# Optimization experiments

Hardware: AMD Instinct MI355X
Metric: run time of the kernel (lower is better)

The kernel has to match this reference:

```python
import jax, jax.numpy as jnp
import numpy as np

EPS = 1e-8  # `eps` is an undefined global in the original repo snippet; standard capsule eps
CH_J, N_J, R_NUM = 32, 4, 3


def _squash(s):
    # Faithful to the source: norm / (1 + norm^2 + eps) * s, norm over last dim (size 1 here)
    norm = jnp.sqrt(jnp.sum(s * s, axis=-1, keepdims=True))
    return norm / (1.0 + norm ** 2 + EPS) * s


def _unif_act_wt_entropy(k):
    # k: (b, W, W, 1, ch_j, ch_i); softmax was taken over (W, W, ch_j) per (b, ch_i).
    # Entropy of coupling coefficients normalized by uniform entropy, averaged.
    b, ci = k.shape[0], k.shape[-1]
    p = jnp.transpose(k, (0, 5, 3, 1, 2, 4)).reshape(b, ci, -1)
    ent = -jnp.sum(p * jnp.log(p + EPS), axis=-1)
    return jnp.mean(ent / jnp.log(jnp.asarray(p.shape[-1], p.dtype)))


def reference(inputs, conv_w, conv_b):
    b, ch_i, n_i, h, w = inputs.shape
    # (b, 1, ch_i*n_i, h, w) -> Conv3d stride (n_i,1,1), pad (0,1,1)
    x = inputs.reshape(b, 1, ch_i * n_i, h, w)
    x = jax.lax.conv_general_dilated(
        x, conv_w, window_strides=(n_i, 1, 1),
        padding=((0, 0), (1, 1), (1, 1)),
        dimension_numbers=('NCDHW', 'OIDHW', 'NCDHW'))
    x = x + conv_b[None, :, None, None, None]
    W = x.shape[-1]
    # (b, ch_i, ch_j*n_j, W, W) -> (b, W, W, n_j, ch_j, ch_i)
    x = jnp.transpose(x, (0, 2, 1, 3, 4)).reshape(b, ch_i, CH_J, N_J, W, W)
    x = jnp.transpose(x, (0, 4, 5, 3, 2, 1))

    B = jnp.zeros((b, W, W, 1, CH_J, ch_i), dtype=x.dtype)
    S_hat = None
    k = None
    for i in range(R_NUM):
        # softmax over (W, W, ch_j) jointly, per (b, ch_i)
        logits = jnp.transpose(B, (0, 5, 3, 1, 2, 4)).reshape(b, ch_i, 1, -1)
        k = jax.nn.softmax(logits, axis=-1)
        k = jnp.transpose(k.reshape(b, ch_i, 1, W, W, CH_J), (0, 3, 4, 2, 5, 1))
        S = jnp.sum(k * x, axis=-1, keepdims=True)  # (b, W, W, n_j, ch_j, 1)
        S_hat = _squash(S)
        if i < R_NUM - 1:
            B = B + jnp.sum(S_hat * x, axis=3, keepdims=True)

    out = jnp.transpose(S_hat[..., 0], (0, 4, 3, 1, 2))  # (b, ch_j, n_j, W, W)
    return out, _unif_act_wt_entropy(k)


def setup_inputs() -> dict:
    key = jax.random.key(0)
    k1, k2, k3 = jax.random.split(key, 3)
    inputs = jax.random.normal(k1, (8, 32, 8, 32, 32), dtype=jnp.float32)
    conv_w = jax.random.normal(k2, (128, 1, 3, 3, 3), dtype=jnp.float32) * 0.05
    conv_b = jax.random.normal(k3, (128,), dtype=jnp.float32) * 0.05
    return {"inputs": inputs, "conv_w": conv_w, "conv_b": conv_b}
```

## Files before the change

### kernel.cpp

```cpp
#include <hip/hip_runtime.h>
#include <hip/hip_bf16.h>

#define EPSF 1e-8f

typedef short bf16x8 __attribute__((ext_vector_type(8)));
typedef float f32x4 __attribute__((ext_vector_type(4)));


__device__ __forceinline__ float bflo(unsigned u){ return __uint_as_float(u<<16); }
__device__ __forceinline__ float bfhi(unsigned u){ return __uint_as_float(u&0xffff0000u); }
__device__ __forceinline__ float bfu16(unsigned short u){ return __uint_as_float((unsigned)u<<16); }
__device__ __forceinline__ unsigned bfpack2(float a,float b){
    return (__float_as_uint(a)>>16)|(__float_as_uint(b)&0xffff0000u);
}
__device__ __forceinline__ unsigned short bfr16(float a){
    return (unsigned short)(__float_as_uint(a)>>16);
}
__device__ __forceinline__ float fastrcp(float x){ return __builtin_amdgcn_rcpf(x); }
__device__ __forceinline__ bf16x8 pack8(const float* v){
    union { unsigned u[4]; bf16x8 v8; } cv;
#pragma unroll
    for (int j = 0; j < 4; ++j) cv.u[j] = bfpack2(v[2*j], v[2*j+1]);
    return cv.v8;
}

template<int PHASE>
__global__ __launch_bounds__(256, 5) void k_caps(
    const float* __restrict__ in, const float* __restrict__ cw,
    const float* __restrict__ cb, unsigned* __restrict__ Bpk,
    const float* __restrict__ sm_in, const float* __restrict__ siz_in,
    float* __restrict__ pm, float* __restrict__ ps, float* __restrict__ pt,
    float* __restrict__ outp) {
    __shared__ __align__(16) unsigned char smem[29568];
    unsigned short* slabB = (unsigned short*)smem;
    unsigned short* wLT = (unsigned short*)(smem + 6912);
    float* cbL  = (float*)(smem + 14336);
    float* smL  = (float*)(smem + 14848);
    float* sizL = (float*)(smem + 14976);
    unsigned* ktab = (unsigned*)(smem + 15104);

    const int t = threadIdx.x;
    const int lane = t & 63, wid = t >> 6;
    const int bid = blockIdx.x;
    const int bh = bid >> 3, b = bh >> 5, h = bh & 31;
    const int w0 = (bid & 7) << 2;
    const int l15 = lane & 15, lq = lane >> 4;

    unsigned char* wb = smem + 15232 + (size_t)wid * 3584;
    unsigned* Bu  = (unsigned*)wb;
    float* shL    = (float*)(wb + 2560);
    float* auxL   = (float*)(wb + 3072);
    float* statb  = (float*)(wb + 3200);

    for (int j = t; j < 864; j += 256) {
        const int r = j / 3, q = j - r * 3;
        const int ci2 = r / 9, rem = r - ci2 * 9, kd = rem / 3, dy = rem - kd * 3;
        const int y = h + dy - 1;
        const int x0 = w0 - 4 + q * 4;
        float4 f = {0.f, 0.f, 0.f, 0.f};
        if ((unsigned)y < 32u && (unsigned)x0 < 32u)
            f = *reinterpret_cast<const float4*>(
                in + (((size_t)(b * 32 + ci2) * 8 + kd) * 32 + y) * 32 + x0);
        unsigned* sp = (unsigned*)slabB + r * 6 + q * 2;
        sp[0] = bfpack2(f.x, f.y);
        sp[1] = bfpack2(f.z, f.w);
    }
    for (int j = t; j < 3456; j += 256) {
        const int c = j / 27, k = j - c * 27;
        wLT[k * 132 + c] = bfr16(cw[j]);
    }
    if (t < 128) cbL[t] = cb[t];
    if (t < 32) {
        const int k = t < 27 ? t : 26;
        const int kd = k / 9, r9 = k - kd * 9, dy = r9 / 3, dx = r9 - dy * 3;
        ktab[t] = (unsigned)((kd * 3 + dy) * 12 + dx);
    }
    if constexpr (PHASE >= 1) {
        if (t < 32) { smL[t] = sm_in[b * 32 + t]; sizL[t] = siz_in[b * 32 + t]; }
    }
    __syncthreads();

    const size_t loc = (size_t)bh * 32 + w0 + wid;
    const int tb = wid + 3;

    float b1v[16];
    if constexpr (PHASE == 0) {
        const int k2 = lane >> 1, half = lane & 1;
        float vs = 0.f;
        if (k2 < 27) {
            const unsigned short* sp = slabB + half * 16 * 108 + ktab[k2] + tb;
#pragma unroll
            for (int i = 0; i < 16; ++i) vs += bfu16(sp[i * 108]);
        }
        vs += __shfl_xor(vs, 1);
        if (half == 0 && k2 < 27) auxL[k2] = vs;
    } else {
        const uint4* Bg = (const uint4*)(Bpk + loc * 512 + (size_t)lane * 8);
        const uint4 q0 = Bg[0], q1 = Bg[1];
        const unsigned pk[8] = {q0.x, q0.y, q0.z, q0.w, q1.x, q1.y, q1.z, q1.w};
#pragma unroll
        for (int e = 0; e < 8; ++e) { b1v[2*e] = bflo(pk[e]); b1v[2*e+1] = bfhi(pk[e]); }
#pragma unroll
        for (int mt = 0; mt < 2; ++mt)
#pragma unroll
        for (int reg = 0; reg < 4; ++reg)
#pragma unroll
        for (int nt = 0; nt < 2; ++nt) {
            const float me = b1v[mt*8 + nt*4 + reg];
            const float ot = __shfl_xor(me, 1);
            const unsigned pku = (l15 & 1) ? bfpack2(ot, me) : bfpack2(me, ot);
            if ((l15 & 1) == nt)
                Bu[(mt*16 + lq*4 + reg)*20 + nt*8 + (l15 >> 1)] = pku;
        }
        bf16x8 kmA[2];
#pragma unroll
        for (int mt = 0; mt < 2; ++mt) {
            const uint4 q = *(const uint4*)(Bu + (mt*16 + l15)*20 + lq*4);
            const unsigned uu[4] = {q.x, q.y, q.z, q.w};
            float ev[8];
#pragma unroll
            for (int j2 = 0; j2 < 4; ++j2) {
                const int ci0 = lq*8 + 2*j2;
                ev[2*j2]   = __expf(bflo(uu[j2]) - smL[ci0])   * sizL[ci0];
                ev[2*j2+1] = __expf(bfhi(uu[j2]) - smL[ci0+1]) * sizL[ci0+1];
            }
            kmA[mt] = pack8(ev);
        }
        bf16x8 vtB[2];
#pragma unroll
        for (int nt = 0; nt < 2; ++nt) {
            const int kt = nt*16 + l15;
            const unsigned ko = ktab[kt];
            union { unsigned short s[8]; bf16x8 v8; } cv;
#pragma unroll
            for (int j = 0; j < 8; ++j) {
                const unsigned short sv = slabB[(lq*8 + j)*108 + ko + tb];
                cv.s[j] = (kt < 27) ? sv : (unsigned short)(kt == 27 ? 0x3f80 : 0);
            }
            vtB[nt] = cv.v8;
        }
        f32x4 accu[2][2];
#pragma unroll
        for (int mt = 0; mt < 2; ++mt)
#pragma unroll
        for (int nt = 0; nt < 2; ++nt)
            accu[mt][nt] = __builtin_amdgcn_mfma_f32_16x16x32_bf16(
                kmA[mt], vtB[nt], (f32x4){0.f,0.f,0.f,0.f}, 0, 0, 0);
#pragma unroll
        for (int mt = 0; mt < 2; ++mt)
#pragma unroll
        for (int reg = 0; reg < 4; ++reg)
#pragma unroll
        for (int nt = 0; nt < 2; ++nt) {
            const float me = accu[mt][nt][reg];
            const float ot = __shfl_xor(me, 1);
            const unsigned pku = (l15 & 1) ? bfpack2(ot, me) : bfpack2(me, ot);
            if ((l15 & 1) == nt)
                Bu[(mt*16 + lq*4 + reg)*20 + nt*8 + (l15 >> 1)] = pku;
        }
    }

#pragma unroll
    for (int cc = 0; cc < 2; ++cc) {
        const int c = lane + cc * 64;
        float S;
        if constexpr (PHASE == 0) {
            S = 0.f;
#pragma unroll
            for (int k = 0; k < 27; ++k)
                S = fmaf(bfu16(wLT[k*132 + c]), auxL[k], S);
            S = S * (1.0f/32768.0f) + cbL[c] * (1.0f/1024.0f);
        } else {
            const unsigned* up = Bu + (c >> 2) * 20;
            S = 0.f;
#pragma unroll
            for (int p = 0; p < 13; ++p) {
                const unsigned u = up[p];
                S = fmaf(bfu16(wLT[(2*p)*132 + c]),   bflo(u), S);
                S = fmaf(bfu16(wLT[(2*p+1)*132 + c]), bfhi(u), S);
            }
            const unsigned u13 = up[13];
            S = fmaf(bfu16(wLT[26*132 + c]), bflo(u13), S);
            S = fmaf(cbL[c], bfhi(u13), S);
        }
        const float sq = fabsf(S) * S * fastrcp(1.f + S*S + EPSF);
        shL[c] = sq;
    }

    if constexpr (PHASE == 2) {
        __syncthreads();
        if (t < 128) {
            const float* s0 = (const float*)(smem + 15232 + 0*3584 + 2560);
            const float* s1 = (const float*)(smem + 15232 + 1*3584 + 2560);
            const float* s2 = (const float*)(smem + 15232 + 2*3584 + 2560);
            const float* s3 = (const float*)(smem + 15232 + 3*3584 + 2560);
            float4 o = make_float4(s0[t], s1[t], s2[t], s3[t]);
            *reinterpret_cast<float4*>(
                outp + ((size_t)(b*128 + t))*1024 + (size_t)h*32 + w0) = o;
        }
        if (bid == 0) {
            float* er = (float*)smem;
            er[t] = pt[t];
            __syncthreads();
            for (int s2v = 128; s2v > 0; s2v >>= 1) {
                if (t < s2v) er[t] += er[t + s2v];
                __syncthreads();
            }
            if (t == 0) outp[1048576] = er[0] * (1.0f/256.0f);
        }
        return;
    }

    {
        const int k0 = 2*l15, k1 = k0 + 1;
#pragma unroll
        for (int i = 0; i < 8; ++i) {
            const int cj = lq + 4*i;
            float v0 = 0.f, v1 = 0.f;
            if (k0 < 27) {
#pragma unroll
                for (int nj = 0; nj < 4; ++nj)
                    v0 = fmaf(shL[cj*4+nj], bfu16(wLT[k0*132 + cj*4 + nj]), v0);
            }
            if (k1 < 27) {
#pragma unroll
                for (int nj = 0; nj < 4; ++nj)
                    v1 = fmaf(shL[cj*4+nj], bfu16(wLT[k1*132 + cj*4 + nj]), v1);
            }
            Bu[cj*20 + l15] = bfpack2(v0, v1);
        }
        if (lane < 32) {
            float cv = 0.f;
#pragma unroll
            for (int nj = 0; nj < 4; ++nj)
                cv = fmaf(shL[lane*4+nj], cbL[lane*4+nj], cv);
            auxL[lane] = cv;
        }
    }

    bf16x8 wsA[2], vB[2];
#pragma unroll
    for (int mt = 0; mt < 2; ++mt) {
        union { uint4 q4; bf16x8 v8; } cv;
        cv.q4 = *(const uint4*)(Bu + (mt*16 + l15)*20 + lq*4);
        wsA[mt] = cv.v8;
    }
#pragma unroll
    for (int nt = 0; nt < 2; ++nt) {
        const int ci = nt*16 + l15;
        union { unsigned short s[8]; bf16x8 v8; } cv;
#pragma unroll
        for (int j = 0; j < 8; ++j) {
            const int k = lq*8 + j;
            const unsigned short sv = slabB[ci*108 + ktab[k] + tb];
            cv.s[j] = (k < 27) ? sv : (unsigned short)0;
        }
        vB[nt] = cv.v8;
    }
    f32x4 accb[2][2];
#pragma unroll
    for (int mt = 0; mt < 2; ++mt)
#pragma unroll
    for (int nt = 0; nt < 2; ++nt)
        accb[mt][nt] = __builtin_amdgcn_mfma_f32_16x16x32_bf16(
            wsA[mt], vB[nt], (f32x4){0.f,0.f,0.f,0.f}, 0, 0, 0);

    float bnew[16];
#pragma unroll
    for (int mt = 0; mt < 2; ++mt)
#pragma unroll
    for (int nt = 0; nt < 2; ++nt)
#pragma unroll
    for (int reg = 0; reg < 4; ++reg) {
        float val = accb[mt][nt][reg] + auxL[mt*16 + lq*4 + reg];
        if constexpr (PHASE == 1) val += b1v[mt*8 + nt*4 + reg];
        bnew[mt*8 + nt*4 + reg] = val;
    }
    {
        unsigned pk[8];
#pragma unroll
        for (int e = 0; e < 8; ++e) pk[e] = bfpack2(bnew[2*e], bnew[2*e+1]);
        uint4* Bg = (uint4*)(Bpk + loc * 512 + (size_t)lane * 8);
        Bg[0] = make_uint4(pk[0], pk[1], pk[2], pk[3]);
        Bg[1] = make_uint4(pk[4], pk[5], pk[6], pk[7]);
    }
    float m2[2], s2[2], T2[2];
#pragma unroll
    for (int nt = 0; nt < 2; ++nt) {
        float m = -1e30f;
#pragma unroll
        for (int mt = 0; mt < 2; ++mt)
#pragma unroll
        for (int reg = 0; reg < 4; ++reg) m = fmaxf(m, bnew[mt*8 + nt*4 + reg]);
        float s = 0.f, T = 0.f;
#pragma unroll
        for (int mt = 0; mt < 2; ++mt)
#pragma unroll
        for (int reg = 0; reg < 4; ++reg) {
            const float d = bnew[mt*8 + nt*4 + reg] - m;
            const float e = __expf(d);
            s += e; T += e * d;
        }
        m2[nt] = m; s2[nt] = s; T2[nt] = T;
#pragma unroll
        for (int off = 16; off <= 32; off <<= 1) {
            const float mo = __shfl_xor(m2[nt], off);
            const float so = __shfl_xor(s2[nt], off);
            const float To = __shfl_xor(T2[nt], off);
            const float nm = fmaxf(m2[nt], mo);
            const float ea = __expf(m2[nt]-nm), eb = __expf(mo-nm);
            T2[nt] = ea*(T2[nt] + s2[nt]*(m2[nt]-nm)) + eb*(To + so*(mo-nm));
            s2[nt] = ea*s2[nt] + eb*so;
            m2[nt] = nm;
        }
    }
    if (lane < 16) {
#pragma unroll
        for (int nt = 0; nt < 2; ++nt) {
            const int ci = nt*16 + lane;
            statb[ci] = m2[nt]; statb[32+ci] = s2[nt]; statb[64+ci] = T2[nt];
        }
    }
    __syncthreads();
    if (t < 32) {
        float M = -1e30f, Z = 0.f, T = 0.f;
#pragma unroll
        for (int wv = 0; wv < 4; ++wv) {
            const float* sw = (const float*)(smem + 15232 + wv*3584 + 3200);
            const float mo = sw[t], so = sw[32+t], To = sw[64+t];
            const float nm = fmaxf(M, mo);
            const float ea = __expf(M-nm), eb = __expf(mo-nm);
            T = ea*(T + Z*(M-nm)) + eb*(To + so*(mo-nm));
            Z = ea*Z + eb*so;
            M = nm;
        }
        pm[bid*32 + t] = M;
        ps[bid*32 + t] = Z;
        if constexpr (PHASE == 1) pt[bid*32 + t] = T;
    }
}

template <int NPART, bool ENT>
__global__ __launch_bounds__(256) void k_comb(const float* __restrict__ pm,
                                              const float* __restrict__ ps,
                                              const float* __restrict__ pt,
                                              float* __restrict__ sm,
                                              float* __restrict__ siz,
                                              float* __restrict__ entp) {
    const int b = blockIdx.x, t = threadIdx.x;
    const int ci = t & 31, seg = t >> 5;
    constexpr int PER = NPART / 8;
    __shared__ float red[3][8][33];

    float M = -1e30f;
    for (int k = 0; k < PER; ++k)
        M = fmaxf(M, pm[((size_t)b * NPART + seg * PER + k) * 32 + ci]);
    red[0][seg][ci] = M;
    __syncthreads();
    float Mg = red[0][0][ci];
#pragma unroll
    for (int q = 1; q < 8; ++q) Mg = fmaxf(Mg, red[0][q][ci]);

    float Z = 0.0f, T = 0.0f;
    for (int k = 0; k < PER; ++k) {
        const size_t i = ((size_t)b * NPART + seg * PER + k) * 32 + ci;
        const float dm = pm[i] - Mg;
        const float e = __expf(dm);
        Z += ps[i] * e;
        if constexpr (ENT) T += (pt[i] + ps[i] * dm) * e;
    }
    red[1][seg][ci] = Z;
    if constexpr (ENT) red[2][seg][ci] = T;
    __syncthreads();
    if (t < 32) {
        float Zt = 0.0f, Tt = 0.0f;
#pragma unroll
        for (int q = 0; q < 8; ++q) {
            Zt += red[1][q][ci];
            if constexpr (ENT) Tt += red[2][q][ci];
        }
        sm[b * 32 + ci] = Mg;
        siz[b * 32 + ci] = 1.0f / Zt;
        if constexpr (ENT)
            entp[b * 32 + ci] = (logf(Zt) - Tt / Zt) * (1.0f / 10.39720770839918f);
    }
}

extern "C" void kernel_launch(void* const* d_in, const int* in_sizes, int n_in,
                              void* d_out, int out_size, void* d_ws, size_t ws_size,
                              hipStream_t stream) {
    const float* in = (const float*)d_in[0];
    const float* cw = (const float*)d_in[1];
    const float* cb = (const float*)d_in[2];
    float* out = (float*)d_out;

    unsigned* Bpk = (unsigned*)d_ws;
    float* pm0  = (float*)(Bpk + 4194304);
    float* ps0  = pm0 + 65536;
    float* pm1  = ps0 + 65536;
    float* ps1  = pm1 + 65536;
    float* pt1  = ps1 + 65536;
    float* sm0  = pt1 + 65536;
    float* siz0 = sm0 + 256;
    float* sm1  = siz0 + 256;
    float* siz1 = sm1 + 256;
    float* entp = siz1 + 256;

    k_caps<0><<<2048, 256, 0, stream>>>(in, cw, cb, Bpk, sm0, siz0, pm0, ps0, pt1, out);
    k_comb<256, false><<<8, 256, 0, stream>>>(pm0, ps0, nullptr, sm0, siz0, nullptr);
    k_caps<1><<<2048, 256, 0, stream>>>(in, cw, cb, Bpk, sm0, siz0, pm1, ps1, pt1, out);
    k_comb<256, true><<<8, 256, 0, stream>>>(pm1, ps1, pt1, sm1, siz1, entp);
    k_caps<2><<<2048, 256, 0, stream>>>(in, cw, cb, Bpk, sm1, siz1, pm1, ps1, entp, out);
}
```

Before: 85.61 us.

## Fold softmax-stat combine kernels into caps phases and widen tiles to 8 columns

Removes the two small k_comb launches by having each k_caps phase reduce the previous phase's per-block partial max/sum statistics itself at block start. Each block now covers 8 output columns (two per wave, looped) instead of 4, so the grid halves, the slab is wider and the number of partials per batch halves. Phase 2 computes the entropy from the raw partials in block 0. The intent is to cut launch and serialization overhead and to amortize slab and weight staging over more work. In exchange every block repeats the combine reduction, LDS use grows, and per-wave work is serialized over two columns.

```diff
diff --git a/kernel.cpp b/kernel.cpp
--- a/kernel.cpp
+++ b/kernel.cpp
@@ -28,32 +28,61 @@
 __global__ __launch_bounds__(256, 5) void k_caps(
     const float* __restrict__ in, const float* __restrict__ cw,
     const float* __restrict__ cb, unsigned* __restrict__ Bpk,
-    const float* __restrict__ sm_in, const float* __restrict__ siz_in,
-    float* __restrict__ pm, float* __restrict__ ps, float* __restrict__ pt,
+    const float* __restrict__ pmi, const float* __restrict__ psi,
+    const float* __restrict__ pti,
+    float* __restrict__ pmo, float* __restrict__ pso, float* __restrict__ pto,
     float* __restrict__ outp) {
-    __shared__ __align__(16) unsigned char smem[29568];
+    __shared__ __align__(16) unsigned char smem[31872];
     unsigned short* slabB = (unsigned short*)smem;
-    unsigned short* wLT = (unsigned short*)(smem + 6912);
-    float* cbL  = (float*)(smem + 14336);
-    float* smL  = (float*)(smem + 14848);
-    float* sizL = (float*)(smem + 14976);
-    unsigned* ktab = (unsigned*)(smem + 15104);
+    unsigned short* wLT = (unsigned short*)(smem + 9216);
+    float* cbL  = (float*)(smem + 16640);
+    float* smL  = (float*)(smem + 17152);
+    float* sizL = (float*)(smem + 17280);
+    unsigned* ktab = (unsigned*)(smem + 17408);
 
     const int t = threadIdx.x;
     const int lane = t & 63, wid = t >> 6;
     const int bid = blockIdx.x;
-    const int bh = bid >> 3, b = bh >> 5, h = bh & 31;
-    const int w0 = (bid & 7) << 2;
+    const int bh = bid >> 2, b = bid >> 7, h = bh & 31;
+    const int w0 = (bid & 3) << 3;
     const int l15 = lane & 15, lq = lane >> 4;
 
-    unsigned char* wb = smem + 15232 + (size_t)wid * 3584;
+    unsigned char* wb = smem + 17536 + (size_t)wid * 3584;
     unsigned* Bu  = (unsigned*)wb;
     float* shL    = (float*)(wb + 2560);
     float* auxL   = (float*)(wb + 3072);
     float* statb  = (float*)(wb + 3200);
 
-    for (int j = t; j < 864; j += 256) {
-        const int r = j / 3, q = j - r * 3;
+    if constexpr (PHASE >= 1) {
+        const int seg = t >> 5, ci = t & 31;
+        float M = -1e30f, Z = 0.f;
+#pragma unroll 4
+        for (int j = 0; j < 16; ++j) {
+            const int idx = (b * 128 + seg * 16 + j) * 32 + ci;
+            const float m = pmi[idx], s = psi[idx];
+            const float nm = fmaxf(M, m);
+            Z = Z * __expf(M - nm) + s * __expf(m - nm);
+            M = nm;
+        }
+        float* comb = (float*)smem;
+        comb[seg * 32 + ci] = M; comb[256 + seg * 32 + ci] = Z;
+        __syncthreads();
+        if (t < 32) {
+            float Mg = -1e30f, Zg = 0.f;
+#pragma unroll
+            for (int q = 0; q < 8; ++q) {
+                const float m = comb[q * 32 + t], s = comb[256 + q * 32 + t];
+                const float nm = fmaxf(Mg, m);
+                Zg = Zg * __expf(Mg - nm) + s * __expf(m - nm);
+                Mg = nm;
+            }
+            smL[t] = Mg; sizL[t] = 1.0f / Zg;
+        }
+        __syncthreads();
+    }
+
+    for (int j = t; j < 1152; j += 256) {
+        const int r = j >> 2, q = j & 3;
         const int ci2 = r / 9, rem = r - ci2 * 9, kd = rem / 3, dy = rem - kd * 3;
         const int y = h + dy - 1;
         const int x0 = w0 - 4 + q * 4;
@@ -61,7 +90,7 @@
         if ((unsigned)y < 32u && (unsigned)x0 < 32u)
             f = *reinterpret_cast<const float4*>(
                 in + (((size_t)(b * 32 + ci2) * 8 + kd) * 32 + y) * 32 + x0);
-        unsigned* sp = (unsigned*)slabB + r * 6 + q * 2;
+        unsigned* sp = (unsigned*)slabB + r * 8 + q * 2;
         sp[0] = bfpack2(f.x, f.y);
         sp[1] = bfpack2(f.z, f.w);
     }
@@ -73,134 +102,250 @@
     if (t < 32) {
         const int k = t < 27 ? t : 26;
         const int kd = k / 9, r9 = k - kd * 9, dy = r9 / 3, dx = r9 - dy * 3;
-        ktab[t] = (unsigned)((kd * 3 + dy) * 12 + dx);
-    }
-    if constexpr (PHASE >= 1) {
-        if (t < 32) { smL[t] = sm_in[b * 32 + t]; sizL[t] = siz_in[b * 32 + t]; }
+        ktab[t] = (unsigned)((kd * 3 + dy) * 16 + dx);
     }
     __syncthreads();
 
-    const size_t loc = (size_t)bh * 32 + w0 + wid;
-    const int tb = wid + 3;
-
-    float b1v[16];
-    if constexpr (PHASE == 0) {
-        const int k2 = lane >> 1, half = lane & 1;
-        float vs = 0.f;
-        if (k2 < 27) {
-            const unsigned short* sp = slabB + half * 16 * 108 + ktab[k2] + tb;
-#pragma unroll
-            for (int i = 0; i < 16; ++i) vs += bfu16(sp[i * 108]);
-        }
-        vs += __shfl_xor(vs, 1);
-        if (half == 0 && k2 < 27) auxL[k2] = vs;
-    } else {
-        const uint4* Bg = (const uint4*)(Bpk + loc * 512 + (size_t)lane * 8);
-        const uint4 q0 = Bg[0], q1 = Bg[1];
-        const unsigned pk[8] = {q0.x, q0.y, q0.z, q0.w, q1.x, q1.y, q1.z, q1.w};
-#pragma unroll
-        for (int e = 0; e < 8; ++e) { b1v[2*e] = bflo(pk[e]); b1v[2*e+1] = bfhi(pk[e]); }
+    float MwA[2] = {-1e30f, -1e30f}, SwA[2] = {0.f, 0.f}, TwA[2] = {0.f, 0.f};
+
+#pragma unroll 1
+    for (int L = 0; L < 2; ++L) {
+        const int wl = wid * 2 + L;
+        const size_t loc = (size_t)bh * 32 + w0 + wl;
+        const int tb = wl + 3;
+
+        float b1v[16];
+        if constexpr (PHASE == 0) {
+            const int k2 = lane >> 1, half = lane & 1;
+            float vs = 0.f;
+            if (k2 < 27) {
+                const unsigned short* sp = slabB + half * 16 * 144 + ktab[k2] + tb;
+#pragma unroll
+                for (int i = 0; i < 16; ++i) vs += bfu16(sp[i * 144]);
+            }
+            vs += __shfl_xor(vs, 1);
+            if (half == 0 && k2 < 27) auxL[k2] = vs;
+        } else {
+            const uint4* Bg = (const uint4*)(Bpk + loc * 512 + (size_t)lane * 8);
+            const uint4 q0 = Bg[0], q1 = Bg[1];
+            const unsigned pk[8] = {q0.x, q0.y, q0.z, q0.w, q1.x, q1.y, q1.z, q1.w};
+#pragma unroll
+            for (int e = 0; e < 8; ++e) { b1v[2*e] = bflo(pk[e]); b1v[2*e+1] = bfhi(pk[e]); }
+#pragma unroll
+            for (int mt = 0; mt < 2; ++mt)
+#pragma unroll
+            for (int reg = 0; reg < 4; ++reg)
+#pragma unroll
+            for (int nt = 0; nt < 2; ++nt) {
+                const float me = b1v[mt*8 + nt*4 + reg];
+                const float ot = __shfl_xor(me, 1);
+                const unsigned pku = (l15 & 1) ? bfpack2(ot, me) : bfpack2(me, ot);
+                if ((l15 & 1) == nt)
+                    Bu[(mt*16 + lq*4 + reg)*20 + nt*8 + (l15 >> 1)] = pku;
+            }
+            bf16x8 kmA[2];
+#pragma unroll
+            for (int mt = 0; mt < 2; ++mt) {
+                const uint4 q = *(const uint4*)(Bu + (mt*16 + l15)*20 + lq*4);
+                const unsigned uu[4] = {q.x, q.y, q.z, q.w};
+                float ev[8];
+#pragma unroll
+                for (int j2 = 0; j2 < 4; ++j2) {
+                    const int ci0 = lq*8 + 2*j2;
+                    ev[2*j2]   = __expf(bflo(uu[j2]) - smL[ci0])   * sizL[ci0];
+                    ev[2*j2+1] = __expf(bfhi(uu[j2]) - smL[ci0+1]) * sizL[ci0+1];
+                }
+                kmA[mt] = pack8(ev);
+            }
+            bf16x8 vtB[2];
+#pragma unroll
+            for (int nt = 0; nt < 2; ++nt) {
+                const int kt = nt*16 + l15;
+                const unsigned ko = ktab[kt];
+                union { unsigned short s[8]; bf16x8 v8; } cv;
+#pragma unroll
+                for (int j = 0; j < 8; ++j) {
+                    const unsigned short sv = slabB[(lq*8 + j)*144 + ko + tb];
+                    cv.s[j] = (kt < 27) ? sv : (unsigned short)(kt == 27 ? 0x3f80 : 0);
+                }
+                vtB[nt] = cv.v8;
+            }
+            f32x4 accu[2][2];
+#pragma unroll
+            for (int mt = 0; mt < 2; ++mt)
+#pragma unroll
+            for (int nt = 0; nt < 2; ++nt)
+                accu[mt][nt] = __builtin_amdgcn_mfma_f32_16x16x32_bf16(
+                    kmA[mt], vtB[nt], (f32x4){0.f,0.f,0.f,0.f}, 0, 0, 0);
+#pragma unroll
+            for (int mt = 0; mt < 2; ++mt)
+#pragma unroll
+            for (int reg = 0; reg < 4; ++reg)
+#pragma unroll
+            for (int nt = 0; nt < 2; ++nt) {
+                const float me = accu[mt][nt][reg];
+                const float ot = __shfl_xor(me, 1);
+                const unsigned pku = (l15 & 1) ? bfpack2(ot, me) : bfpack2(me, ot);
+                if ((l15 & 1) == nt)
+                    Bu[(mt*16 + lq*4 + reg)*20 + nt*8 + (l15 >> 1)] = pku;
+            }
+        }
+
+#pragma unroll
+        for (int cc = 0; cc < 2; ++cc) {
+            const int c = lane + cc * 64;
+            float S;
+            if constexpr (PHASE == 0) {
+                S = 0.f;
+#pragma unroll
+                for (int k = 0; k < 27; ++k)
+                    S = fmaf(bfu16(wLT[k*132 + c]), auxL[k], S);
+                S = S * (1.0f/32768.0f) + cbL[c] * (1.0f/1024.0f);
+            } else {
+                const unsigned* up = Bu + (c >> 2) * 20;
+                S = 0.f;
+#pragma unroll
+                for (int p = 0; p < 13; ++p) {
+                    const unsigned u = up[p];
+                    S = fmaf(bfu16(wLT[(2*p)*132 + c]),   bflo(u), S);
+                    S = fmaf(bfu16(wLT[(2*p+1)*132 + c]), bfhi(u), S);
+                }
+                const unsigned u13 = up[13];
+                S = fmaf(bfu16(wLT[26*132 + c]), bflo(u13), S);
+                S = fmaf(cbL[c], bfhi(u13), S);
+            }
+            const float sq = fabsf(S) * S * fastrcp(1.f + S*S + EPSF);
+            if constexpr (PHASE == 2) shL[L * 128 + c] = sq;
+            else shL[c] = sq;
+        }
+        if constexpr (PHASE == 2) continue;
+
+        {
+            const int k0 = 2*l15, k1 = k0 + 1;
+#pragma unroll
+            for (int i = 0; i < 8; ++i) {
+                const int cj = lq + 4*i;
+                float v0 = 0.f, v1 = 0.f;
+                if (k0 < 27) {
+#pragma unroll
+                    for (int nj = 0; nj < 4; ++nj)
+                        v0 = fmaf(shL[cj*4+nj], bfu16(wLT[k0*132 + cj*4 + nj]), v0);
+                }
+                if (k1 < 27) {
+#pragma unroll
+                    for (int nj = 0; nj < 4; ++nj)
+                        v1 = fmaf(shL[cj*4+nj], bfu16(wLT[k1*132 + cj*4 + nj]), v1);
+                }
+                Bu[cj*20 + l15] = bfpack2(v0, v1);
+            }
+            if (lane < 32) {
+                float cv = 0.f;
+#pragma unroll
+                for (int nj = 0; nj < 4; ++nj)
+                    cv = fmaf(shL[lane*4+nj], cbL[lane*4+nj], cv);
+                auxL[lane] = cv;
+            }
+        }
+
+        bf16x8 wsA[2], vB[2];
+#pragma unroll
+        for (int mt = 0; mt < 2; ++mt) {
+            union { uint4 q4; bf16x8 v8; } cv;
+            cv.q4 = *(const uint4*)(Bu + (mt*16 + l15)*20 + lq*4);
+            wsA[mt] = cv.v8;
+        }
+#pragma unroll
+        for (int nt = 0; nt < 2; ++nt) {
+            const int ci = nt*16 + l15;
+            union { unsigned short s[8]; bf16x8 v8; } cv;
+#pragma unroll
+            for (int j = 0; j < 8; ++j) {
+                const int k = lq*8 + j;
+                const unsigned short sv = slabB[ci*144 + ktab[k] + tb];
+                cv.s[j] = (k < 27) ? sv : (unsigned short)0;
+            }
+            vB[nt] = cv.v8;
+        }
+        f32x4 accb[2][2];
 #pragma unroll
         for (int mt = 0; mt < 2; ++mt)
 #pragma unroll
-        for (int reg = 0; reg < 4; ++reg)
+        for (int nt = 0; nt < 2; ++nt)
+            accb[mt][nt] = __builtin_amdgcn_mfma_f32_16x16x32_bf16(
+                wsA[mt], vB[nt], (f32x4){0.f,0.f,0.f,0.f}, 0, 0, 0);
+
+        float bnew[16];
+#pragma unroll
+        for (int mt = 0; mt < 2; ++mt)
+#pragma unroll
+        for (int nt = 0; nt < 2; ++nt)
+#pragma unroll
+        for (int reg = 0; reg < 4; ++reg) {
+            float val = accb[mt][nt][reg] + auxL[mt*16 + lq*4 + reg];
+            if constexpr (PHASE == 1) val += b1v[mt*8 + nt*4 + reg];
+            bnew[mt*8 + nt*4 + reg] = val;
+        }
+        {
+            unsigned pk[8];
+#pragma unroll
+            for (int e = 0; e < 8; ++e) pk[e] = bfpack2(bnew[2*e], bnew[2*e+1]);
+            uint4* Bg = (uint4*)(Bpk + loc * 512 + (size_t)lane * 8);
+            Bg[0] = make_uint4(pk[0], pk[1], pk[2], pk[3]);
+            Bg[1] = make_uint4(pk[4], pk[5], pk[6], pk[7]);
+        }
 #pragma unroll
         for (int nt = 0; nt < 2; ++nt) {
-            const float me = b1v[mt*8 + nt*4 + reg];
-            const float ot = __shfl_xor(me, 1);
-            const unsigned pku = (l15 & 1) ? bfpack2(ot, me) : bfpack2(me, ot);
-            if ((l15 & 1) == nt)
-                Bu[(mt*16 + lq*4 + reg)*20 + nt*8 + (l15 >> 1)] = pku;
-        }
-        bf16x8 kmA[2];
-#pragma unroll
-        for (int mt = 0; mt < 2; ++mt) {
-            const uint4 q = *(const uint4*)(Bu + (mt*16 + l15)*20 + lq*4);
-            const unsigned uu[4] = {q.x, q.y, q.z, q.w};
-            float ev[8];
-#pragma unroll
-            for (int j2 = 0; j2 < 4; ++j2) {
-                const int ci0 = lq*8 + 2*j2;
-                ev[2*j2]   = __expf(bflo(uu[j2]) - smL[ci0])   * sizL[ci0];
-                ev[2*j2+1] = __expf(bfhi(uu[j2]) - smL[ci0+1]) * sizL[ci0+1];
-            }
-            kmA[mt] = pack8(ev);
-        }
-        bf16x8 vtB[2];
-#pragma unroll
-        for (int nt = 0; nt < 2; ++nt) {
-            const int kt = nt*16 + l15;
-            const unsigned ko = ktab[kt];
-            union { unsigned short s[8]; bf16x8 v8; } cv;
-#pragma unroll
-            for (int j = 0; j < 8; ++j) {
-                const unsigned short sv = slabB[(lq*8 + j)*108 + ko + tb];
-                cv.s[j] = (kt < 27) ? sv : (unsigned short)(kt == 27 ? 0x3f80 : 0);
-            }
-            vtB[nt] = cv.v8;
-        }
-        f32x4 accu[2][2];
-#pragma unroll
-        for (int mt = 0; mt < 2; ++mt)
-#pragma unroll
-        for (int nt = 0; nt < 2; ++nt)
-            accu[mt][nt] = __builtin_amdgcn_mfma_f32_16x16x32_bf16(
-                kmA[mt], vtB[nt], (f32x4){0.f,0.f,0.f,0.f}, 0, 0, 0);
-#pragma unroll
-        for (int mt = 0; mt < 2; ++mt)
-#pragma unroll
-        for (int reg = 0; reg < 4; ++reg)
-#pragma unroll
-        for (int nt = 0; nt < 2; ++nt) {
-            const float me = accu[mt][nt][reg];
-            const float ot = __shfl_xor(me, 1);
-            const unsigned pku = (l15 & 1) ? bfpack2(ot, me) : bfpack2(me, ot);
-            if ((l15 & 1) == nt)
-                Bu[(mt*16 + lq*4 + reg)*20 + nt*8 + (l15 >> 1)] = pku;
-        }
-    }
-
-#pragma unroll
-    for (int cc = 0; cc < 2; ++cc) {
-        const int c = lane + cc * 64;
-        float S;
-        if constexpr (PHASE == 0) {
-            S = 0.f;
-#pragma unroll
-            for (int k = 0; k < 27; ++k)
-                S = fmaf(bfu16(wLT[k*132 + c]), auxL[k], S);
-            S = S * (1.0f/32768.0f) + cbL[c] * (1.0f/1024.0f);
-        } else {
-            const unsigned* up = Bu + (c >> 2) * 20;
-            S = 0.f;
-#pragma unroll
-            for (int p = 0; p < 13; ++p) {
-                const unsigned u = up[p];
-                S = fmaf(bfu16(wLT[(2*p)*132 + c]),   bflo(u), S);
-                S = fmaf(bfu16(wLT[(2*p+1)*132 + c]), bfhi(u), S);
-            }
-            const unsigned u13 = up[13];
-            S = fmaf(bfu16(wLT[26*132 + c]), bflo(u13), S);
-            S = fmaf(cbL[c], bfhi(u13), S);
-        }
-        const float sq = fabsf(S) * S * fastrcp(1.f + S*S + EPSF);
-        shL[c] = sq;
+            float m = -1e30f;
+#pragma unroll
+            for (int mt = 0; mt < 2; ++mt)
+#pragma unroll
+            for (int reg = 0; reg < 4; ++reg) m = fmaxf(m, bnew[mt*8 + nt*4 + reg]);
+            float s = 0.f, T = 0.f;
+#pragma unroll
+            for (int mt = 0; mt < 2; ++mt)
+#pragma unroll
+            for (int reg = 0; reg < 4; ++reg) {
+                const float d = bnew[mt*8 + nt*4 + reg] - m;
+                const float e = __expf(d);
+                s += e; T += e * d;
+            }
+            const float nm = fmaxf(MwA[nt], m);
+            const float ea = __expf(MwA[nt]-nm), eb = __expf(m-nm);
+            TwA[nt] = ea*(TwA[nt] + SwA[nt]*(MwA[nt]-nm)) + eb*(T + s*(m-nm));
+            SwA[nt] = ea*SwA[nt] + eb*s;
+            MwA[nt] = nm;
+        }
     }
 
     if constexpr (PHASE == 2) {
         __syncthreads();
-        if (t < 128) {
-            const float* s0 = (const float*)(smem + 15232 + 0*3584 + 2560);
-            const float* s1 = (const float*)(smem + 15232 + 1*3584 + 2560);
-            const float* s2 = (const float*)(smem + 15232 + 2*3584 + 2560);
-            const float* s3 = (const float*)(smem + 15232 + 3*3584 + 2560);
-            float4 o = make_float4(s0[t], s1[t], s2[t], s3[t]);
+        {
+            const int c = t >> 1, w4 = (t & 1) * 4;
+            float o[4];
+#pragma unroll
+            for (int j = 0; j < 4; ++j) {
+                const int w = w4 + j;
+                o[j] = ((const float*)(smem + 17536 + (w >> 1) * 3584 + 2560))
+                           [(w & 1) * 128 + c];
+            }
             *reinterpret_cast<float4*>(
-                outp + ((size_t)(b*128 + t))*1024 + (size_t)h*32 + w0) = o;
+                outp + ((size_t)(b*128 + c))*1024 + (size_t)h*32 + w0) =
+                make_float4(o[0], o[1], o[2], o[3]);
         }
         if (bid == 0) {
+            const int bb = t >> 5, ci = t & 31;
+            float M = -1e30f, Z = 0.f, T = 0.f;
+            for (int j = 0; j < 128; ++j) {
+                const int idx = (bb * 128 + j) * 32 + ci;
+                const float mo = pmi[idx], so = psi[idx], To = pti[idx];
+                const float nm = fmaxf(M, mo);
+                const float ea = __expf(M-nm), eb = __expf(mo-nm);
+                T = ea*(T + Z*(M-nm)) + eb*(To + so*(mo-nm));
+                Z = ea*Z + eb*so;
+                M = nm;
+            }
             float* er = (float*)smem;
-            er[t] = pt[t];
+            er[t] = (logf(Z) - T/Z) * (1.0f/10.39720770839918f);
             __syncthreads();
             for (int s2v = 128; s2v > 0; s2v >>= 1) {
                 if (t < s2v) er[t] += er[t + s2v];
@@ -211,114 +356,25 @@
         return;
     }
 
-    {
-        const int k0 = 2*l15, k1 = k0 + 1;
-#pragma unroll
-        for (int i = 0; i < 8; ++i) {
-            const int cj = lq + 4*i;
-            float v0 = 0.f, v1 = 0.f;
-            if (k0 < 27) {
-#pragma unroll
-                for (int nj = 0; nj < 4; ++nj)
-                    v0 = fmaf(shL[cj*4+nj], bfu16(wLT[k0*132 + cj*4 + nj]), v0);
-            }
-            if (k1 < 27) {
-#pragma unroll
-                for (int nj = 0; nj < 4; ++nj)
-                    v1 = fmaf(shL[cj*4+nj], bfu16(wLT[k1*132 + cj*4 + nj]), v1);
-            }
-            Bu[cj*20 + l15] = bfpack2(v0, v1);
-        }
-        if (lane < 32) {
-            float cv = 0.f;
-#pragma unroll
-            for (int nj = 0; nj < 4; ++nj)
-                cv = fmaf(shL[lane*4+nj], cbL[lane*4+nj], cv);
-            auxL[lane] = cv;
-        }
-    }
-
-    bf16x8 wsA[2], vB[2];
-#pragma unroll
-    for (int mt = 0; mt < 2; ++mt) {
-        union { uint4 q4; bf16x8 v8; } cv;
-        cv.q4 = *(const uint4*)(Bu + (mt*16 + l15)*20 + lq*4);
-        wsA[mt] = cv.v8;
-    }
 #pragma unroll
     for (int nt = 0; nt < 2; ++nt) {
-        const int ci = nt*16 + l15;
-        union { unsigned short s[8]; bf16x8 v8; } cv;
-#pragma unroll
-        for (int j = 0; j < 8; ++j) {
-            const int k = lq*8 + j;
-            const unsigned short sv = slabB[ci*108 + ktab[k] + tb];
-            cv.s[j] = (k < 27) ? sv : (unsigned short)0;
-        }
-        vB[nt] = cv.v8;
-    }
-    f32x4 accb[2][2];
-#pragma unroll
-    for (int mt = 0; mt < 2; ++mt)
-#pragma unroll
-    for (int nt = 0; nt < 2; ++nt)
-        accb[mt][nt] = __builtin_amdgcn_mfma_f32_16x16x32_bf16(
-            wsA[mt], vB[nt], (f32x4){0.f,0.f,0.f,0.f}, 0, 0, 0);
-
-    float bnew[16];
-#pragma unroll
-    for (int mt = 0; mt < 2; ++mt)
-#pragma unroll
-    for (int nt = 0; nt < 2; ++nt)
-#pragma unroll
-    for (int reg = 0; reg < 4; ++reg) {
-        float val = accb[mt][nt][reg] + auxL[mt*16 + lq*4 + reg];
-        if constexpr (PHASE == 1) val += b1v[mt*8 + nt*4 + reg];
-        bnew[mt*8 + nt*4 + reg] = val;
-    }
-    {
-        unsigned pk[8];
-#pragma unroll
-        for (int e = 0; e < 8; ++e) pk[e] = bfpack2(bnew[2*e], bnew[2*e+1]);
-        uint4* Bg = (uint4*)(Bpk + loc * 512 + (size_t)lane * 8);
-        Bg[0] = make_uint4(pk[0], pk[1], pk[2], pk[3]);
-        Bg[1] = make_uint4(pk[4], pk[5], pk[6], pk[7]);
-    }
-    float m2[2], s2[2], T2[2];
-#pragma unroll
-    for (int nt = 0; nt < 2; ++nt) {
-        float m = -1e30f;
-#pragma unroll
-        for (int mt = 0; mt < 2; ++mt)
-#pragma unroll
-        for (int reg = 0; reg < 4; ++reg) m = fmaxf(m, bnew[mt*8 + nt*4 + reg]);
-        float s = 0.f, T = 0.f;
-#pragma unroll
-        for (int mt = 0; mt < 2; ++mt)
-#pragma unroll
-        for (int reg = 0; reg < 4; ++reg) {
-            const float d = bnew[mt*8 + nt*4 + reg] - m;
-            const float e = __expf(d);
-            s += e; T += e * d;
-        }
-        m2[nt] = m; s2[nt] = s; T2[nt] = T;
 #pragma unroll
         for (int off = 16; off <= 32; off <<= 1) {
-            const float mo = __shfl_xor(m2[nt], off);
-            const float so = __shfl_xor(s2[nt], off);
-            const float To = __shfl_xor(T2[nt], off);
-            const float nm = fmaxf(m2[nt], mo);
-            const float ea = __expf(m2[nt]-nm), eb = __expf(mo-nm);
-            T2[nt] = ea*(T2[nt] + s2[nt]*(m2[nt]-nm)) + eb*(To + so*(mo-nm));
-            s2[nt] = ea*s2[nt] + eb*so;
-            m2[nt] = nm;
+            const float mo = __shfl_xor(MwA[nt], off);
+            const float so = __shfl_xor(SwA[nt], off);
+            const float To = __shfl_xor(TwA[nt], off);
+            const float nm = fmaxf(MwA[nt], mo);
+            const float ea = __expf(MwA[nt]-nm), eb = __expf(mo-nm);
+            TwA[nt] = ea*(TwA[nt] + SwA[nt]*(MwA[nt]-nm)) + eb*(To + so*(mo-nm));
+            SwA[nt] = ea*SwA[nt] + eb*so;
+            MwA[nt] = nm;
         }
     }
     if (lane < 16) {
 #pragma unroll
         for (int nt = 0; nt < 2; ++nt) {
             const int ci = nt*16 + lane;
-            statb[ci] = m2[nt]; statb[32+ci] = s2[nt]; statb[64+ci] = T2[nt];
+            statb[ci] = MwA[nt]; statb[32+ci] = SwA[nt]; statb[64+ci] = TwA[nt];
         }
     }
     __syncthreads();
@@ -326,7 +382,7 @@
         float M = -1e30f, Z = 0.f, T = 0.f;
 #pragma unroll
         for (int wv = 0; wv < 4; ++wv) {
-            const float* sw = (const float*)(smem + 15232 + wv*3584 + 3200);
+            const float* sw = (const float*)(smem + 17536 + wv*3584 + 3200);
             const float mo = sw[t], so = sw[32+t], To = sw[64+t];
             const float nm = fmaxf(M, mo);
             const float ea = __expf(M-nm), eb = __expf(mo-nm);
@@ -334,55 +390,9 @@
             Z = ea*Z + eb*so;
             M = nm;
         }
-        pm[bid*32 + t] = M;
-        ps[bid*32 + t] = Z;
-        if constexpr (PHASE == 1) pt[bid*32 + t] = T;
-    }
-}
-
-template <int NPART, bool ENT>
-__global__ __launch_bounds__(256) void k_comb(const float* __restrict__ pm,
-                                              const float* __restrict__ ps,
-                                              const float* __restrict__ pt,
-                                              float* __restrict__ sm,
-                                              float* __restrict__ siz,
-                                              float* __restrict__ entp) {
-    const int b = blockIdx.x, t = threadIdx.x;
-    const int ci = t & 31, seg = t >> 5;
-    constexpr int PER = NPART / 8;
-    __shared__ float red[3][8][33];
-
-    float M = -1e30f;
-    for (int k = 0; k < PER; ++k)
-        M = fmaxf(M, pm[((size_t)b * NPART + seg * PER + k) * 32 + ci]);
-    red[0][seg][ci] = M;
-    __syncthreads();
-    float Mg = red[0][0][ci];
-#pragma unroll
-    for (int q = 1; q < 8; ++q) Mg = fmaxf(Mg, red[0][q][ci]);
-
-    float Z = 0.0f, T = 0.0f;
-    for (int k = 0; k < PER; ++k) {
-        const size_t i = ((size_t)b * NPART + seg * PER + k) * 32 + ci;
-        const float dm = pm[i] - Mg;
-        const float e = __expf(dm);
-        Z += ps[i] * e;
-        if constexpr (ENT) T += (pt[i] + ps[i] * dm) * e;
-    }
-    red[1][seg][ci] = Z;
-    if constexpr (ENT) red[2][seg][ci] = T;
-    __syncthreads();
-    if (t < 32) {
-        float Zt = 0.0f, Tt = 0.0f;
-#pragma unroll
-        for (int q = 0; q < 8; ++q) {
-            Zt += red[1][q][ci];
-            if constexpr (ENT) Tt += red[2][q][ci];
-        }
-        sm[b * 32 + ci] = Mg;
-        siz[b * 32 + ci] = 1.0f / Zt;
-        if constexpr (ENT)
-            entp[b * 32 + ci] = (logf(Zt) - Tt / Zt) * (1.0f / 10.39720770839918f);
+        pmo[bid*32 + t] = M;
+        pso[bid*32 + t] = Z;
+        if constexpr (PHASE == 1) pto[bid*32 + t] = T;
     }
 }
 
@@ -396,19 +406,18 @@
 
     unsigned* Bpk = (unsigned*)d_ws;
     float* pm0  = (float*)(Bpk + 4194304);
-    float* ps0  = pm0 + 65536;
-    float* pm1  = ps0 + 65536;
-    float* ps1  = pm1 + 65536;
-    float* pt1  = ps1 + 65536;
-    float* sm0  = pt1 + 65536;
-    float* siz0 = sm0 + 256;
-    float* sm1  = siz0 + 256;
-    float* siz1 = sm1 + 256;
-    float* entp = siz1 + 256;
-
-    k_caps<0><<<2048, 256, 0, stream>>>(in, cw, cb, Bpk, sm0, siz0, pm0, ps0, pt1, out);
-    k_comb<256, false><<<8, 256, 0, stream>>>(pm0, ps0, nullptr, sm0, siz0, nullptr);
-    k_caps<1><<<2048, 256, 0, stream>>>(in, cw, cb, Bpk, sm0, siz0, pm1, ps1, pt1, out);
-    k_comb<256, true><<<8, 256, 0, stream>>>(pm1, ps1, pt1, sm1, siz1, entp);
-    k_caps<2><<<2048, 256, 0, stream>>>(in, cw, cb, Bpk, sm1, siz1, pm1, ps1, entp, out);
+    float* ps0  = pm0 + 32768;
+    float* pm1  = ps0 + 32768;
+    float* ps1  = pm1 + 32768;
+    float* pt1  = ps1 + 32768;
+
+    k_caps<0><<<1024, 256, 0, stream>>>(in, cw, cb, Bpk,
+                                        nullptr, nullptr, nullptr,
+                                        pm0, ps0, pt1, out);
+    k_caps<1><<<1024, 256, 0, stream>>>(in, cw, cb, Bpk,
+                                        pm0, ps0, nullptr,
+                                        pm1, ps1, pt1, out);
+    k_caps<2><<<1024, 256, 0, stream>>>(in, cw, cb, Bpk,
+                                        pm1, ps1, pt1,
+                                        nullptr, nullptr, nullptr, out);
 }
```

Measured after the change: 170.5 us. +99.2%, slower.

## Fold softmax partial combine into consumer caps kernels, drop k_comb launches

Applied to the files above, without the earlier changes.

Removes the two small k_comb launches and instead has every block of the next caps phase redundantly reduce the 256 per-block partial max/sum values for its batch at kernel start. The phase-2 block 0 also recomputes the entropy combine serially. This saves two kernel launches and their serialization gaps, at the cost of each of 2048 blocks reading 16K floats and doing online-softmax merging up front, plus a long serial 256-step loop in block 0.

```diff
diff --git a/kernel.cpp b/kernel.cpp
--- a/kernel.cpp
+++ b/kernel.cpp
@@ -28,8 +28,9 @@
 __global__ __launch_bounds__(256, 5) void k_caps(
     const float* __restrict__ in, const float* __restrict__ cw,
     const float* __restrict__ cb, unsigned* __restrict__ Bpk,
-    const float* __restrict__ sm_in, const float* __restrict__ siz_in,
-    float* __restrict__ pm, float* __restrict__ ps, float* __restrict__ pt,
+    const float* __restrict__ pmi, const float* __restrict__ psi,
+    const float* __restrict__ pti,
+    float* __restrict__ pmo, float* __restrict__ pso, float* __restrict__ pto,
     float* __restrict__ outp) {
     __shared__ __align__(16) unsigned char smem[29568];
     unsigned short* slabB = (unsigned short*)smem;
@@ -51,6 +52,34 @@
     float* shL    = (float*)(wb + 2560);
     float* auxL   = (float*)(wb + 3072);
     float* statb  = (float*)(wb + 3200);
+
+    if constexpr (PHASE >= 1) {
+        const int seg = t >> 5, ci = t & 31;
+        float M = -1e30f, Z = 0.f;
+#pragma unroll 4
+        for (int j = 0; j < 32; ++j) {
+            const int idx = (b * 256 + seg * 32 + j) * 32 + ci;
+            const float m = pmi[idx], s = psi[idx];
+            const float nm = fmaxf(M, m);
+            Z = Z * __expf(M - nm) + s * __expf(m - nm);
+            M = nm;
+        }
+        float* comb = (float*)smem;
+        comb[seg * 32 + ci] = M; comb[256 + seg * 32 + ci] = Z;
+        __syncthreads();
+        if (t < 32) {
+            float Mg = -1e30f, Zg = 0.f;
+#pragma unroll
+            for (int q = 0; q < 8; ++q) {
+                const float m = comb[q * 32 + t], s = comb[256 + q * 32 + t];
+                const float nm = fmaxf(Mg, m);
+                Zg = Zg * __expf(Mg - nm) + s * __expf(m - nm);
+                Mg = nm;
+            }
+            smL[t] = Mg; sizL[t] = 1.0f / Zg;
+        }
+        __syncthreads();
+    }
 
     for (int j = t; j < 864; j += 256) {
         const int r = j / 3, q = j - r * 3;
@@ -75,9 +104,6 @@
         const int kd = k / 9, r9 = k - kd * 9, dy = r9 / 3, dx = r9 - dy * 3;
         ktab[t] = (unsigned)((kd * 3 + dy) * 12 + dx);
     }
-    if constexpr (PHASE >= 1) {
-        if (t < 32) { smL[t] = sm_in[b * 32 + t]; sizL[t] = siz_in[b * 32 + t]; }
-    }
     __syncthreads();
 
     const size_t loc = (size_t)bh * 32 + w0 + wid;
@@ -199,8 +225,20 @@
                 outp + ((size_t)(b*128 + t))*1024 + (size_t)h*32 + w0) = o;
         }
         if (bid == 0) {
+            const int bb = t >> 5, ci = t & 31;
+            float M = -1e30f, Z = 0.f, T = 0.f;
+            for (int j = 0; j < 256; ++j) {
+                const int idx = (bb * 256 + j) * 32 + ci;
+                const float mo = pmi[idx], so = psi[idx], To = pti[idx];
+                const float nm = fmaxf(M, mo);
+                const float ea = __expf(M-nm), eb = __expf(mo-nm);
+                T = ea*(T + Z*(M-nm)) + eb*(To + so*(mo-nm));
+                Z = ea*Z + eb*so;
+                M = nm;
+            }
+            __syncthreads();
             float* er = (float*)smem;
-            er[t] = pt[t];
+            er[t] = (logf(Z) - T/Z) * (1.0f/10.39720770839918f);
             __syncthreads();
             for (int s2v = 128; s2v > 0; s2v >>= 1) {
                 if (t < s2v) er[t] += er[t + s2v];
@@ -334,55 +372,9 @@
             Z = ea*Z + eb*so;
             M = nm;
         }
-        pm[bid*32 + t] = M;
-        ps[bid*32 + t] = Z;
-        if constexpr (PHASE == 1) pt[bid*32 + t] = T;
-    }
-}
-
-template <int NPART, bool ENT>
-__global__ __launch_bounds__(256) void k_comb(const float* __restrict__ pm,
-                                              const float* __restrict__ ps,
-                                              const float* __restrict__ pt,
-                                              float* __restrict__ sm,
-                                              float* __restrict__ siz,
-                                              float* __restrict__ entp) {
-    const int b = blockIdx.x, t = threadIdx.x;
-    const int ci = t & 31, seg = t >> 5;
-    constexpr int PER = NPART / 8;
-    __shared__ float red[3][8][33];
-
-    float M = -1e30f;
-    for (int k = 0; k < PER; ++k)
-        M = fmaxf(M, pm[((size_t)b * NPART + seg * PER + k) * 32 + ci]);
-    red[0][seg][ci] = M;
-    __syncthreads();
-    float Mg = red[0][0][ci];
-#pragma unroll
-    for (int q = 1; q < 8; ++q) Mg = fmaxf(Mg, red[0][q][ci]);
-
-    float Z = 0.0f, T = 0.0f;
-    for (int k = 0; k < PER; ++k) {
-        const size_t i = ((size_t)b * NPART + seg * PER + k) * 32 + ci;
-        const float dm = pm[i] - Mg;
-        const float e = __expf(dm);
-        Z += ps[i] * e;
-        if constexpr (ENT) T += (pt[i] + ps[i] * dm) * e;
-    }
-    red[1][seg][ci] = Z;
-    if constexpr (ENT) red[2][seg][ci] = T;
-    __syncthreads();
-    if (t < 32) {
-        float Zt = 0.0f, Tt = 0.0f;
-#pragma unroll
-        for (int q = 0; q < 8; ++q) {
-            Zt += red[1][q][ci];
-            if constexpr (ENT) Tt += red[2][q][ci];
-        }
-        sm[b * 32 + ci] = Mg;
-        siz[b * 32 + ci] = 1.0f / Zt;
-        if constexpr (ENT)
-            entp[b * 32 + ci] = (logf(Zt) - Tt / Zt) * (1.0f / 10.39720770839918f);
+        pmo[bid*32 + t] = M;
+        pso[bid*32 + t] = Z;
+        if constexpr (PHASE == 1) pto[bid*32 + t] = T;
     }
 }
 
@@ -400,15 +392,14 @@
     float* pm1  = ps0 + 65536;
     float* ps1  = pm1 + 65536;
     float* pt1  = ps1 + 65536;
-    float* sm0  = pt1 + 65536;
-    float* siz0 = sm0 + 256;
-    float* sm1  = siz0 + 256;
-    float* siz1 = sm1 + 256;
-    float* entp = siz1 + 256;
-
-    k_caps<0><<<2048, 256, 0, stream>>>(in, cw, cb, Bpk, sm0, siz0, pm0, ps0, pt1, out);
-    k_comb<256, false><<<8, 256, 0, stream>>>(pm0, ps0, nullptr, sm0, siz0, nullptr);
-    k_caps<1><<<2048, 256, 0, stream>>>(in, cw, cb, Bpk, sm0, siz0, pm1, ps1, pt1, out);
-    k_comb<256, true><<<8, 256, 0, stream>>>(pm1, ps1, pt1, sm1, siz1, entp);
-    k_caps<2><<<2048, 256, 0, stream>>>(in, cw, cb, Bpk, sm1, siz1, pm1, ps1, entp, out);
+
+    k_caps<0><<<2048, 256, 0, stream>>>(in, cw, cb, Bpk,
+                                        nullptr, nullptr, nullptr,
+                                        pm0, ps0, pt1, out);
+    k_caps<1><<<2048, 256, 0, stream>>>(in, cw, cb, Bpk,
+                                        pm0, ps0, nullptr,
+                                        pm1, ps1, pt1, out);
+    k_caps<2><<<2048, 256, 0, stream>>>(in, cw, cb, Bpk,
+                                        pm1, ps1, pt1,
+                                        nullptr, nullptr, nullptr, out);
 }
```

Measured after the change: 98.66 us. 1.15x slower.

## Precompute bf16 weights once, shrink LDS slab and per-wave buffers for occupancy

Applied to the files above, without the earlier changes.

A new one-block prep kernel converts and transposes the conv weights to bf16 in workspace, so each k_caps block copies them with vector loads instead of converting 3456 floats. The input slab now stores only the 8 columns actually needed (stride 72 instead of 108), and the per-wave stat buffer aliases the squash buffer, cutting LDS from about 29.5 KB to 25.7 KB. Launch bounds are raised to 6 blocks per CU to use the freed LDS. This adds an extra kernel launch and relies on statb/shL aliasing being safe in every phase.

```diff
diff --git a/kernel.cpp b/kernel.cpp
--- a/kernel.cpp
+++ b/kernel.cpp
@@ -24,20 +24,29 @@
     return cv.v8;
 }
 
+__global__ __launch_bounds__(256) void k_prep(const float* __restrict__ cw,
+                                              unsigned short* __restrict__ wg) {
+    const int t = threadIdx.x;
+    for (int j = t; j < 3456; j += 256) {
+        const int c = j / 27, k = j - c * 27;
+        wg[k * 132 + c] = bfr16(cw[j]);
+    }
+}
+
 template<int PHASE>
-__global__ __launch_bounds__(256, 5) void k_caps(
-    const float* __restrict__ in, const float* __restrict__ cw,
+__global__ __launch_bounds__(256, 6) void k_caps(
+    const float* __restrict__ in, const unsigned short* __restrict__ wg,
     const float* __restrict__ cb, unsigned* __restrict__ Bpk,
     const float* __restrict__ sm_in, const float* __restrict__ siz_in,
     float* __restrict__ pm, float* __restrict__ ps, float* __restrict__ pt,
     float* __restrict__ outp) {
-    __shared__ __align__(16) unsigned char smem[29568];
+    __shared__ __align__(16) unsigned char smem[25728];
     unsigned short* slabB = (unsigned short*)smem;
-    unsigned short* wLT = (unsigned short*)(smem + 6912);
-    float* cbL  = (float*)(smem + 14336);
-    float* smL  = (float*)(smem + 14848);
-    float* sizL = (float*)(smem + 14976);
-    unsigned* ktab = (unsigned*)(smem + 15104);
+    unsigned short* wLT = (unsigned short*)(smem + 4608);
+    float* cbL  = (float*)(smem + 12032);
+    float* smL  = (float*)(smem + 12544);
+    float* sizL = (float*)(smem + 12672);
+    unsigned* ktab = (unsigned*)(smem + 12800);
 
     const int t = threadIdx.x;
     const int lane = t & 63, wid = t >> 6;
@@ -46,11 +55,11 @@
     const int w0 = (bid & 7) << 2;
     const int l15 = lane & 15, lq = lane >> 4;
 
-    unsigned char* wb = smem + 15232 + (size_t)wid * 3584;
+    unsigned char* wb = smem + 12928 + (size_t)wid * 3200;
     unsigned* Bu  = (unsigned*)wb;
     float* shL    = (float*)(wb + 2560);
     float* auxL   = (float*)(wb + 3072);
-    float* statb  = (float*)(wb + 3200);
+    float* statb  = (float*)(wb + 2560);
 
     for (int j = t; j < 864; j += 256) {
         const int r = j / 3, q = j - r * 3;
@@ -61,19 +70,22 @@
         if ((unsigned)y < 32u && (unsigned)x0 < 32u)
             f = *reinterpret_cast<const float4*>(
                 in + (((size_t)(b * 32 + ci2) * 8 + kd) * 32 + y) * 32 + x0);
-        unsigned* sp = (unsigned*)slabB + r * 6 + q * 2;
-        sp[0] = bfpack2(f.x, f.y);
-        sp[1] = bfpack2(f.z, f.w);
-    }
-    for (int j = t; j < 3456; j += 256) {
-        const int c = j / 27, k = j - c * 27;
-        wLT[k * 132 + c] = bfr16(cw[j]);
+        unsigned* sp = (unsigned*)slabB + r * 4;
+        if (q == 0)      sp[0] = bfpack2(f.z, f.w);
+        else if (q == 1) { sp[1] = bfpack2(f.x, f.y);
+                           sp[2] = bfpack2(f.z, f.w); }
+        else             sp[3] = bfpack2(f.x, f.y);
+    }
+    {
+        const uint4* wg4 = (const uint4*)wg;
+        uint4* wl4 = (uint4*)wLT;
+        for (int j = t; j < 464; j += 256) wl4[j] = wg4[j];
     }
     if (t < 128) cbL[t] = cb[t];
     if (t < 32) {
         const int k = t < 27 ? t : 26;
         const int kd = k / 9, r9 = k - kd * 9, dy = r9 / 3, dx = r9 - dy * 3;
-        ktab[t] = (unsigned)((kd * 3 + dy) * 12 + dx);
+        ktab[t] = (unsigned)((kd * 3 + dy) * 8 + dx);
     }
     if constexpr (PHASE >= 1) {
         if (t < 32) { smL[t] = sm_in[b * 32 + t]; sizL[t] = siz_in[b * 32 + t]; }
@@ -81,16 +93,16 @@
     __syncthreads();
 
     const size_t loc = (size_t)bh * 32 + w0 + wid;
-    const int tb = wid + 3;
+    const int tb = wid + 1;
 
     float b1v[16];
     if constexpr (PHASE == 0) {
         const int k2 = lane >> 1, half = lane & 1;
         float vs = 0.f;
         if (k2 < 27) {
-            const unsigned short* sp = slabB + half * 16 * 108 + ktab[k2] + tb;
-#pragma unroll
-            for (int i = 0; i < 16; ++i) vs += bfu16(sp[i * 108]);
+            const unsigned short* sp = slabB + half * 16 * 72 + ktab[k2] + tb;
+#pragma unroll
+            for (int i = 0; i < 16; ++i) vs += bfu16(sp[i * 72]);
         }
         vs += __shfl_xor(vs, 1);
         if (half == 0 && k2 < 27) auxL[k2] = vs;
@@ -134,7 +146,7 @@
             union { unsigned short s[8]; bf16x8 v8; } cv;
 #pragma unroll
             for (int j = 0; j < 8; ++j) {
-                const unsigned short sv = slabB[(lq*8 + j)*108 + ko + tb];
+                const unsigned short sv = slabB[(lq*8 + j)*72 + ko + tb];
                 cv.s[j] = (kt < 27) ? sv : (unsigned short)(kt == 27 ? 0x3f80 : 0);
             }
             vtB[nt] = cv.v8;
@@ -190,10 +202,10 @@
     if constexpr (PHASE == 2) {
         __syncthreads();
         if (t < 128) {
-            const float* s0 = (const float*)(smem + 15232 + 0*3584 + 2560);
-            const float* s1 = (const float*)(smem + 15232 + 1*3584 + 2560);
-            const float* s2 = (const float*)(smem + 15232 + 2*3584 + 2560);
-            const float* s3 = (const float*)(smem + 15232 + 3*3584 + 2560);
+            const float* s0 = (const float*)(smem + 12928 + 0*3200 + 2560);
+            const float* s1 = (const float*)(smem + 12928 + 1*3200 + 2560);
+            const float* s2 = (const float*)(smem + 12928 + 2*3200 + 2560);
+            const float* s3 = (const float*)(smem + 12928 + 3*3200 + 2560);
             float4 o = make_float4(s0[t], s1[t], s2[t], s3[t]);
             *reinterpret_cast<float4*>(
                 outp + ((size_t)(b*128 + t))*1024 + (size_t)h*32 + w0) = o;
@@ -252,7 +264,7 @@
 #pragma unroll
         for (int j = 0; j < 8; ++j) {
             const int k = lq*8 + j;
-            const unsigned short sv = slabB[ci*108 + ktab[k] + tb];
+            const unsigned short sv = slabB[ci*72 + ktab[k] + tb];
             cv.s[j] = (k < 27) ? sv : (unsigned short)0;
         }
         vB[nt] = cv.v8;
@@ -326,7 +338,7 @@
         float M = -1e30f, Z = 0.f, T = 0.f;
 #pragma unroll
         for (int wv = 0; wv < 4; ++wv) {
-            const float* sw = (const float*)(smem + 15232 + wv*3584 + 3200);
+            const float* sw = (const float*)(smem + 12928 + wv*3200 + 2560);
             const float mo = sw[t], so = sw[32+t], To = sw[64+t];
             const float nm = fmaxf(M, mo);
             const float ea = __expf(M-nm), eb = __expf(mo-nm);
@@ -405,10 +417,15 @@
     float* sm1  = siz0 + 256;
     float* siz1 = sm1 + 256;
     float* entp = siz1 + 256;
-
-    k_caps<0><<<2048, 256, 0, stream>>>(in, cw, cb, Bpk, sm0, siz0, pm0, ps0, pt1, out);
+    unsigned short* wg = (unsigned short*)(entp + 256);
+
+    k_prep<<<1, 256, 0, stream>>>(cw, wg);
+    k_caps<0><<<2048, 256, 0, stream>>>(in, wg, cb, Bpk,
+                                        nullptr, nullptr, pm0, ps0, pt1, out);
     k_comb<256, false><<<8, 256, 0, stream>>>(pm0, ps0, nullptr, sm0, siz0, nullptr);
-    k_caps<1><<<2048, 256, 0, stream>>>(in, cw, cb, Bpk, sm0, siz0, pm1, ps1, pt1, out);
+    k_caps<1><<<2048, 256, 0, stream>>>(in, wg, cb, Bpk,
+                                        sm0, siz0, pm1, ps1, pt1, out);
     k_comb<256, true><<<8, 256, 0, stream>>>(pm1, ps1, pt1, sm1, siz1, entp);
-    k_caps<2><<<2048, 256, 0, stream>>>(in, cw, cb, Bpk, sm1, siz1, pm1, ps1, entp, out);
-}
+    k_caps<2><<<2048, 256, 0, stream>>>(in, wg, cb, Bpk,
+                                        sm1, siz1, pm1, ps1, entp, out);
+}
```

Result: faster. 83.82 us (-2.1%).
